# Kernel tuning notes

Measured on AMD Instinct MI355X. Metric: run time of the kernel, lower is better.

Reference implementation:

```python
import jax, jax.numpy as jnp
import numpy as np

EMBED = 1024
HEADS = 16
HEAD_DIM = EMBED // HEADS
LN_EPS = 1e-5


def setup_inputs() -> dict:
    key = jax.random.key(0)
    ks = jax.random.split(key, 12)
    B, LQ, LK = 2, 2048, 2048
    s = 1.0 / np.sqrt(EMBED)
    inp = {
        "query_seq": jax.random.normal(ks[0], (B, LQ, EMBED), jnp.float32),
        "key_value_seq": jax.random.normal(ks[1], (B, LK, EMBED), jnp.float32),
        "prompt_size": 0,
        "Wq": jax.random.normal(ks[2], (EMBED, EMBED), jnp.float32) * s,
        "bq": jnp.zeros((EMBED,), jnp.float32),
        "Wk": jax.random.normal(ks[3], (EMBED, EMBED), jnp.float32) * s,
        "bk": jnp.zeros((EMBED,), jnp.float32),
        "Wv": jax.random.normal(ks[4], (EMBED, EMBED), jnp.float32) * s,
        "bv": jnp.zeros((EMBED,), jnp.float32),
        "Wo": jax.random.normal(ks[5], (EMBED, EMBED), jnp.float32) * s,
        "bo": jnp.zeros((EMBED,), jnp.float32),
        "ln_gamma": jnp.ones((EMBED,), jnp.float32),
        "ln_beta": jnp.zeros((EMBED,), jnp.float32),
    }
    return inp


def _split_heads(x):
    B, L, _ = x.shape
    return x.reshape(B, L, HEADS, HEAD_DIM).transpose(0, 2, 1, 3)  # [B,H,L,Dh]


def reference(query_seq, key_value_seq, prompt_size, Wq, bq, Wk, bk, Wv, bv, Wo, bo, ln_gamma, ln_beta):
    # projections (torch nn.Linear: x @ W.T + b)
    q = _split_heads(query_seq @ Wq.T + bq)
    k = _split_heads(key_value_seq @ Wk.T + bk)
    v = _split_heads(key_value_seq @ Wv.T + bv)
    # naive attention: full score matrix, softmax over keys
    scores = jnp.einsum("bhqd,bhkd->bhqk", q, k) / np.sqrt(HEAD_DIM).astype(np.float32)
    attn = jax.nn.softmax(scores, axis=-1)
    ctx = jnp.einsum("bhqk,bhkd->bhqd", attn, v)
    B, H, LQ, Dh = ctx.shape
    ctx = ctx.transpose(0, 2, 1, 3).reshape(B, LQ, H * Dh)
    out = ctx @ Wo.T + bo
    # residual + LayerNorm
    x = out + query_seq
    mu = jnp.mean(x, axis=-1, keepdims=True)
    var = jnp.var(x, axis=-1, keepdims=True)
    return (x - mu) * jax.lax.rsqrt(var + LN_EPS) * ln_gamma + ln_beta
```

## Files before the change

kernel.cpp:

```cpp
#include <hip/hip_runtime.h>

typedef unsigned short u16;
typedef unsigned int u32;
typedef __attribute__((ext_vector_type(8))) __bf16 bf16x8;
typedef __attribute__((ext_vector_type(4))) short short4v;
typedef __attribute__((ext_vector_type(4))) float f32x4;
typedef __attribute__((ext_vector_type(16))) float f32x16;

#define EMBED 1024
#define NB 2
#define LQ 2048
#define HEADS 16
#define DH 64
#define QSCALE 0.18033688011112042f

__device__ __forceinline__ u16 f2bf(float f) {
  u32 u = __float_as_uint(f);
  u32 r = (u + 0x7FFFu + ((u >> 16) & 1u)) >> 16;
  return (u16)r;
}

__device__ __forceinline__ void glds16(const void* g, void* l) {
  __builtin_amdgcn_global_load_lds((const __attribute__((address_space(1))) void*)g,
                                   (__attribute__((address_space(3))) void*)l, 16, 0, 0);
}

__device__ __forceinline__ f32x4 mfma16(bf16x8 a, bf16x8 b, f32x4 c) {
  return __builtin_amdgcn_mfma_f32_16x16x32_bf16(a, b, c, 0, 0, 0);
}
__device__ __forceinline__ f32x16 mfma32(bf16x8 a, bf16x8 b, f32x16 c) {
  return __builtin_amdgcn_mfma_f32_32x32x16_bf16(a, b, c, 0, 0, 0);
}
__device__ __forceinline__ f32x16 mfma32x8(short4v a, short4v b, f32x16 c) {
  return __builtin_amdgcn_mfma_f32_32x32x8bf16_1k(a, b, c, 0, 0, 0);
}

__device__ __forceinline__ u32 packbf(float a, float b) {
  return __builtin_amdgcn_perm(__float_as_uint(b), __float_as_uint(a), 0x07060302u);
}

__global__ __launch_bounds__(256) void cast_kernel(
    const float* __restrict__ q, const float* __restrict__ kv,
    const float* __restrict__ wq, const float* __restrict__ wk,
    const float* __restrict__ wv, const float* __restrict__ wo,
    u16* __restrict__ qb, u16* __restrict__ kvb, u16* __restrict__ wqb,
    u16* __restrict__ wkb, u16* __restrict__ wvb, u16* __restrict__ wob) {
  int bid = blockIdx.x;
  const float* src;
  u16* dst;
  long base;
  if (bid < 2048) {
    src = q; dst = qb; base = (long)bid * 2048;
  } else if (bid < 4096) {
    src = kv; dst = kvb; base = (long)(bid - 2048) * 2048;
  } else {
    int wsel = (bid - 4096) >> 9;
    int wb = (bid - 4096) & 511;
    if (wsel == 0) { src = wq; dst = wqb; }
    else if (wsel == 1) { src = wk; dst = wkb; }
    else if (wsel == 2) { src = wv; dst = wvb; }
    else { src = wo; dst = wob; }
    base = (long)wb * 2048;
  }
  long e = base + (long)threadIdx.x * 8;
  float4 f0 = *(const float4*)(src + e);
  float4 f1 = *(const float4*)(src + e + 4);
  uint4 o;
  o.x = (u32)f2bf(f0.x) | ((u32)f2bf(f0.y) << 16);
  o.y = (u32)f2bf(f0.z) | ((u32)f2bf(f0.w) << 16);
  o.z = (u32)f2bf(f1.x) | ((u32)f2bf(f1.y) << 16);
  o.w = (u32)f2bf(f1.z) | ((u32)f2bf(f1.w) << 16);
  *(uint4*)(dst + e) = o;
}

template <int IT>
__device__ __forceinline__ void gemm_core(
    u16* As, u16* Bs, const u16* __restrict__ A, const u16* __restrict__ W,
    const float* __restrict__ bias, const float* __restrict__ resid,
    void* __restrict__ outp, int mode, int bx, int by) {
  const int K = EMBED;
  const int TM = IT * 32;
  const int tid = threadIdx.x;
  const int lane = tid & 63;
  const int wv = tid >> 6;
  const int wm = wv >> 1, wn = wv & 1;
  const int l16 = lane & 15, quad = lane >> 4;
  const long tile_m = (long)bx * TM;
  const long tile_n = (long)by * 128;

  f32x4 z4 = {0.f, 0.f, 0.f, 0.f};
  f32x4 acc[IT][4];
#pragma unroll
  for (int i = 0; i < IT; i++)
#pragma unroll
    for (int j = 0; j < 4; j++) acc[i][j] = z4;

  for (int k0 = 0; k0 < K; k0 += 64) {
#pragma unroll
    for (int it = 0; it < TM / 32; it++) {
      int lin = it * 256 + tid;
      int row = lin >> 3, cc = lin & 7;
      glds16(A + (tile_m + row) * K + k0 + ((cc ^ (row & 7)) << 3), As + lin * 8);
    }
#pragma unroll
    for (int it = 0; it < 4; it++) {
      int lin = it * 256 + tid;
      int row = lin >> 3, cc = lin & 7;
      glds16(W + (tile_n + row) * K + k0 + ((cc ^ (row & 7)) << 3), Bs + lin * 8);
    }
    __syncthreads();
    bf16x8 af[IT][2], bfr[4][2];
#pragma unroll
    for (int i = 0; i < IT; i++) {
      int row = wm * (IT * 16) + i * 16 + l16;
#pragma unroll
      for (int ki = 0; ki < 2; ki++)
        af[i][ki] = *(const bf16x8*)(As + row * 64 + (((ki * 4 + quad) ^ (row & 7)) << 3));
    }
#pragma unroll
    for (int j = 0; j < 4; j++) {
      int row = wn * 64 + j * 16 + l16;
#pragma unroll
      for (int ki = 0; ki < 2; ki++)
        bfr[j][ki] = *(const bf16x8*)(Bs + row * 64 + (((ki * 4 + quad) ^ (row & 7)) << 3));
    }
#pragma unroll
    for (int ki = 0; ki < 2; ki++)
#pragma unroll
      for (int i = 0; i < IT; i++)
#pragma unroll
        for (int j = 0; j < 4; j++) acc[i][j] = mfma16(af[i][ki], bfr[j][ki], acc[i][j]);
    __syncthreads();
  }

#pragma unroll
  for (int j = 0; j < 4; j++) {
    int gn = (int)tile_n + wn * 64 + j * 16 + l16;
    float bv = bias[gn];
#pragma unroll
    for (int i = 0; i < IT; i++) {
      long gm0 = tile_m + wm * (IT * 16) + i * 16 + quad * 4;
      if (mode == 3) {
#pragma unroll
        for (int r = 0; r < 4; r++) {
          long idx = (gm0 + r) * EMBED + gn;
          ((float*)outp)[idx] = acc[i][j][r] + bv + resid[idx];
        }
      } else if (mode == 2) {
        int b = (int)(gm0 >> 11), l = (int)(gm0 & 2047);
        int hh = gn >> 6, dh = gn & 63;
        uint2 pk;
        pk.x = (u32)f2bf(acc[i][j][0] + bv) | ((u32)f2bf(acc[i][j][1] + bv) << 16);
        pk.y = (u32)f2bf(acc[i][j][2] + bv) | ((u32)f2bf(acc[i][j][3] + bv) << 16);
        *(uint2*)((u16*)outp + (long)((b * HEADS + hh) * DH + dh) * LQ + l) = pk;
      } else {
#pragma unroll
        for (int r = 0; r < 4; r++) {
          long gm = gm0 + r;
          float v = acc[i][j][r] + bv;
          if (mode == 0) v *= QSCALE;
          int b = (int)(gm >> 11), l = (int)(gm & 2047);
          int hh = gn >> 6, dh = gn & 63;
          ((u16*)outp)[(long)((b * HEADS + hh) * LQ + l) * DH + dh] = f2bf(v);
        }
      }
    }
  }
}

__global__ __launch_bounds__(256) void qkv_kernel(
    const u16* __restrict__ qb, const u16* __restrict__ kvb,
    const u16* __restrict__ wqb, const u16* __restrict__ wkb, const u16* __restrict__ wvb,
    const float* __restrict__ bq, const float* __restrict__ bk, const float* __restrict__ bv,
    u16* __restrict__ Qh, u16* __restrict__ Kh, u16* __restrict__ Vt) {
  __shared__ u16 As[128 * 64];
  __shared__ u16 Bs[128 * 64];
  if (blockIdx.z == 0)      gemm_core<4>(As, Bs, qb,  wqb, bq, nullptr, Qh, 0, blockIdx.x, blockIdx.y);
  else if (blockIdx.z == 1) gemm_core<4>(As, Bs, kvb, wkb, bk, nullptr, Kh, 1, blockIdx.x, blockIdx.y);
  else                      gemm_core<4>(As, Bs, kvb, wvb, bv, nullptr, Vt, 2, blockIdx.x, blockIdx.y);
}

__global__ __launch_bounds__(256) void oproj_kernel(
    const u16* __restrict__ ctx, const u16* __restrict__ wob,
    const float* __restrict__ bo, const float* __restrict__ resid, float* __restrict__ out) {
  __shared__ u16 As[64 * 64];
  __shared__ u16 Bs[128 * 64];
  gemm_core<2>(As, Bs, ctx, wob, bo, resid, out, 3, blockIdx.x, blockIdx.y);
}

__global__ __launch_bounds__(256, 2) void attn_kernel(
    const u16* __restrict__ Qh, const u16* __restrict__ Kh,
    const u16* __restrict__ Vt, u16* __restrict__ ctx) {
  __shared__ u16 Qs[128 * 64];
  __shared__ u16 KVs[2][2][64 * 64];
  const int tid = threadIdx.x;
  const int lane = tid & 63;
  const int wv = tid >> 6;
  const int l32 = lane & 31, h = lane >> 5;
  const int qt = blockIdx.x, bh = blockIdx.y;
  const long qoff = (long)bh * (LQ * DH) + (long)qt * (128 * DH);
  const long koff = (long)bh * (LQ * DH);
  const long voff = (long)bh * (DH * LQ);
  const int qbase = wv * 32;

#pragma unroll
  for (int it = 0; it < 4; it++) {
    int lin = it * 256 + tid;
    int row = lin >> 3, cc = lin & 7;
    glds16(Qh + qoff + row * 64 + ((cc ^ (row & 7)) << 3), Qs + lin * 8);
  }
#pragma unroll
  for (int it = 0; it < 2; it++) {
    int lin = it * 256 + tid;
    int row = lin >> 3, cc = lin & 7;
    glds16(Kh + koff + (long)row * 64 + ((cc ^ (row & 7)) << 3), KVs[0][0] + lin * 8);
    glds16(Vt + voff + (long)row * LQ + ((cc ^ (row & 7)) << 3), KVs[0][1] + lin * 8);
  }
  __syncthreads();

  bf16x8 bq[4];
  {
    int row = qbase + l32;
#pragma unroll
    for (int ks = 0; ks < 4; ks++)
      bq[ks] = *(const bf16x8*)(Qs + row * 64 + (((ks * 2 + h) ^ (row & 7)) << 3));
  }

  f32x16 z16 = {0.f, 0.f, 0.f, 0.f, 0.f, 0.f, 0.f, 0.f,
                0.f, 0.f, 0.f, 0.f, 0.f, 0.f, 0.f, 0.f};
  f32x16 ot[2];
  ot[0] = z16;
  ot[1] = z16;
  float2 ls2 = {0.f, 0.f};

  for (int kt = 0; kt < 32; kt++) {
    const u16* Ks = KVs[kt & 1][0];
    const u16* Vts = KVs[kt & 1][1];
    if (kt + 1 < 32) {
      u16* Kn = (u16*)KVs[(kt + 1) & 1][0];
      u16* Vn = (u16*)KVs[(kt + 1) & 1][1];
#pragma unroll
      for (int it = 0; it < 2; it++) {
        int lin = it * 256 + tid;
        int row = lin >> 3, cc = lin & 7;
        glds16(Kh + koff + (long)((kt + 1) * 64 + row) * 64 + ((cc ^ (row & 7)) << 3), Kn + lin * 8);
        glds16(Vt + voff + (long)row * LQ + (kt + 1) * 64 + ((cc ^ (row & 7)) << 3), Vn + lin * 8);
      }
    }

    f32x16 st[2];
    st[0] = z16;
    st[1] = z16;
#pragma unroll
    for (int ks = 0; ks < 4; ks++) {
#pragma unroll
      for (int mt = 0; mt < 2; mt++) {
        int row = mt * 32 + l32;
        bf16x8 ak = *(const bf16x8*)(Ks + row * 64 + (((ks * 2 + h) ^ (row & 7)) << 3));
        st[mt] = mfma32(ak, bq[ks], st[mt]);
      }
    }

    uint2 pk[2][4];
#pragma unroll
    for (int mt = 0; mt < 2; mt++) {
#pragma unroll
      for (int g = 0; g < 4; g++) {
        float p0 = exp2f(st[mt][g * 4 + 0]);
        float p1 = exp2f(st[mt][g * 4 + 1]);
        float p2 = exp2f(st[mt][g * 4 + 2]);
        float p3 = exp2f(st[mt][g * 4 + 3]);
        float2 a = {p0, p1}, bb = {p2, p3};
        ls2.x += a.x + bb.x;
        ls2.y += a.y + bb.y;
        pk[mt][g].x = packbf(p0, p1);
        pk[mt][g].y = packbf(p2, p3);
      }
    }

#pragma unroll
    for (int t = 0; t < 8; t++) {
      short4v bp = *(short4v*)&pk[t >> 2][t & 3];
#pragma unroll
      for (int mt2 = 0; mt2 < 2; mt2++) {
        int row = mt2 * 32 + l32;
        short4v av = *(const short4v*)(Vts + row * 64 + (((t ^ (row & 7))) << 3) + 4 * h);
        ot[mt2] = mfma32x8(av, bp, ot[mt2]);
      }
    }
    __syncthreads();
  }

  float lsum = ls2.x + ls2.y;
  lsum += __shfl_xor(lsum, 32);
  float inv = 1.0f / lsum;

  const int b = bh >> 4, head = bh & 15;
  int qrow = qt * 128 + qbase + l32;
  long base = (long)(b * LQ + qrow) * EMBED + head * DH;
#pragma unroll
  for (int mt = 0; mt < 2; mt++) {
#pragma unroll
    for (int g = 0; g < 4; g++) {
      uint2 pkk;
      pkk.x = (u32)f2bf(ot[mt][g * 4 + 0] * inv) | ((u32)f2bf(ot[mt][g * 4 + 1] * inv) << 16);
      pkk.y = (u32)f2bf(ot[mt][g * 4 + 2] * inv) | ((u32)f2bf(ot[mt][g * 4 + 3] * inv) << 16);
      *(uint2*)(ctx + base + mt * 32 + g * 8 + 4 * h) = pkk;
    }
  }
}

__global__ __launch_bounds__(256) void ln_kernel(
    float* __restrict__ x, const float* __restrict__ gamma, const float* __restrict__ beta) {
  __shared__ float red[8];
  const int tid = threadIdx.x;
  const long row = blockIdx.x;
  float4 v = *(const float4*)(x + row * EMBED + tid * 4);
  float s = v.x + v.y + v.z + v.w;
  float sq = v.x * v.x + v.y * v.y + v.z * v.z + v.w * v.w;
#pragma unroll
  for (int off = 1; off < 64; off <<= 1) {
    s += __shfl_xor(s, off);
    sq += __shfl_xor(sq, off);
  }
  if ((tid & 63) == 0) {
    red[(tid >> 6) * 2] = s;
    red[(tid >> 6) * 2 + 1] = sq;
  }
  __syncthreads();
  s = red[0] + red[2] + red[4] + red[6];
  sq = red[1] + red[3] + red[5] + red[7];
  float mu = s * (1.f / EMBED);
  float var = sq * (1.f / EMBED) - mu * mu;
  float rstd = rsqrtf(var + 1e-5f);
  float4 g = *(const float4*)(gamma + tid * 4);
  float4 bt = *(const float4*)(beta + tid * 4);
  float4 ov;
  ov.x = (v.x - mu) * rstd * g.x + bt.x;
  ov.y = (v.y - mu) * rstd * g.y + bt.y;
  ov.z = (v.z - mu) * rstd * g.z + bt.z;
  ov.w = (v.w - mu) * rstd * g.w + bt.w;
  *(float4*)(x + row * EMBED + tid * 4) = ov;
}

extern "C" void kernel_launch(void* const* d_in, const int* in_sizes, int n_in,
                              void* d_out, int out_size, void* d_ws, size_t ws_size,
                              hipStream_t stream) {
  const float* q     = (const float*)d_in[0];
  const float* kv    = (const float*)d_in[1];
  const float* Wq    = (const float*)d_in[3];
  const float* bq    = (const float*)d_in[4];
  const float* Wk    = (const float*)d_in[5];
  const float* bk    = (const float*)d_in[6];
  const float* Wv    = (const float*)d_in[7];
  const float* bv    = (const float*)d_in[8];
  const float* Wo    = (const float*)d_in[9];
  const float* bo    = (const float*)d_in[10];
  const float* gamma = (const float*)d_in[11];
  const float* beta  = (const float*)d_in[12];

  char* ws = (char*)d_ws;
  u16* qb  = (u16*)(ws + (0l  << 20));
  u16* kvb = (u16*)(ws + (8l  << 20));
  u16* wqb = (u16*)(ws + (16l << 20));
  u16* wkb = (u16*)(ws + (18l << 20));
  u16* wvb = (u16*)(ws + (20l << 20));
  u16* wob = (u16*)(ws + (22l << 20));
  u16* Qh  = (u16*)(ws + (24l << 20));
  u16* Kh  = (u16*)(ws + (32l << 20));
  u16* Vt  = (u16*)(ws + (40l << 20));
  u16* ctx = (u16*)(ws + (48l << 20));
  float* out = (float*)d_out;

  cast_kernel<<<6144, 256, 0, stream>>>(q, kv, Wq, Wk, Wv, Wo, qb, kvb, wqb, wkb, wvb, wob);
  qkv_kernel<<<dim3(32, 8, 3), 256, 0, stream>>>(qb, kvb, wqb, wkb, wvb, bq, bk, bv, Qh, Kh, Vt);
  attn_kernel<<<dim3(16, 32), 256, 0, stream>>>(Qh, Kh, Vt, ctx);
  oproj_kernel<<<dim3(64, 8), 256, 0, stream>>>(ctx, wob, bo, q, out);
  ln_kernel<<<4096, 256, 0, stream>>>(out, gamma, beta);
}
```

Before: 242.5 us.

## Split attention over two key halves with a combine kernel for partial sums

Splits the key/value sequence across a new grid dimension so each attention block processes half the keys, writing unnormalized bf16 partial context and row sums; a new combine kernel adds the halves and normalizes. Q staging now reuses the KV shared buffer to cut LDS use, allowing launch bounds of four blocks per CU, and the PV accumulation is split into even/odd accumulators to break MFMA dependency chains. This doubles the grid to improve occupancy and CU fill, at the cost of an extra kernel launch, extra global traffic for partials, and extra bf16 rounding of unnormalized partials. It relies on the absence of a running max, since the two halves share one exponent scale.

```diff
diff --git a/kernel.cpp b/kernel.cpp
--- a/kernel.cpp
+++ b/kernel.cpp
@@ -188,21 +188,21 @@
   gemm_core<2>(As, Bs, ctx, wob, bo, resid, out, 3, blockIdx.x, blockIdx.y);
 }
 
-__global__ __launch_bounds__(256, 2) void attn_kernel(
+__global__ __launch_bounds__(256, 4) void attn_kernel(
     const u16* __restrict__ Qh, const u16* __restrict__ Kh,
-    const u16* __restrict__ Vt, u16* __restrict__ ctx) {
-  __shared__ u16 Qs[128 * 64];
+    const u16* __restrict__ Vt, u16* __restrict__ ctxp, float* __restrict__ lsump) {
   __shared__ u16 KVs[2][2][64 * 64];
   const int tid = threadIdx.x;
   const int lane = tid & 63;
   const int wv = tid >> 6;
   const int l32 = lane & 31, h = lane >> 5;
-  const int qt = blockIdx.x, bh = blockIdx.y;
+  const int qt = blockIdx.x, bh = blockIdx.y, kz = blockIdx.z;
   const long qoff = (long)bh * (LQ * DH) + (long)qt * (128 * DH);
-  const long koff = (long)bh * (LQ * DH);
-  const long voff = (long)bh * (DH * LQ);
+  const long koff = (long)bh * (LQ * DH) + (long)kz * (1024 * DH);
+  const long voff = (long)bh * (DH * LQ) + (long)kz * 1024;
   const int qbase = wv * 32;
 
+  u16* Qs = (u16*)KVs[1];
 #pragma unroll
   for (int it = 0; it < 4; it++) {
     int lin = it * 256 + tid;
@@ -225,18 +225,18 @@
     for (int ks = 0; ks < 4; ks++)
       bq[ks] = *(const bf16x8*)(Qs + row * 64 + (((ks * 2 + h) ^ (row & 7)) << 3));
   }
+  __syncthreads();
 
   f32x16 z16 = {0.f, 0.f, 0.f, 0.f, 0.f, 0.f, 0.f, 0.f,
                 0.f, 0.f, 0.f, 0.f, 0.f, 0.f, 0.f, 0.f};
-  f32x16 ot[2];
-  ot[0] = z16;
-  ot[1] = z16;
+  f32x16 ote[2], oto[2];
+  ote[0] = z16; ote[1] = z16; oto[0] = z16; oto[1] = z16;
   float2 ls2 = {0.f, 0.f};
 
-  for (int kt = 0; kt < 32; kt++) {
+  for (int kt = 0; kt < 16; kt++) {
     const u16* Ks = KVs[kt & 1][0];
     const u16* Vts = KVs[kt & 1][1];
-    if (kt + 1 < 32) {
+    if (kt + 1 < 16) {
       u16* Kn = (u16*)KVs[(kt + 1) & 1][0];
       u16* Vn = (u16*)KVs[(kt + 1) & 1][1];
 #pragma unroll
@@ -270,9 +270,8 @@
         float p1 = exp2f(st[mt][g * 4 + 1]);
         float p2 = exp2f(st[mt][g * 4 + 2]);
         float p3 = exp2f(st[mt][g * 4 + 3]);
-        float2 a = {p0, p1}, bb = {p2, p3};
-        ls2.x += a.x + bb.x;
-        ls2.y += a.y + bb.y;
+        ls2.x += p0 + p2;
+        ls2.y += p1 + p3;
         pk[mt][g].x = packbf(p0, p1);
         pk[mt][g].y = packbf(p2, p3);
       }
@@ -285,7 +284,8 @@
       for (int mt2 = 0; mt2 < 2; mt2++) {
         int row = mt2 * 32 + l32;
         short4v av = *(const short4v*)(Vts + row * 64 + (((t ^ (row & 7))) << 3) + 4 * h);
-        ot[mt2] = mfma32x8(av, bp, ot[mt2]);
+        if (t & 1) oto[mt2] = mfma32x8(av, bp, oto[mt2]);
+        else       ote[mt2] = mfma32x8(av, bp, ote[mt2]);
       }
     }
     __syncthreads();
@@ -293,21 +293,45 @@
 
   float lsum = ls2.x + ls2.y;
   lsum += __shfl_xor(lsum, 32);
-  float inv = 1.0f / lsum;
 
   const int b = bh >> 4, head = bh & 15;
   int qrow = qt * 128 + qbase + l32;
-  long base = (long)(b * LQ + qrow) * EMBED + head * DH;
+  if (h == 0) lsump[((long)kz * 32 + bh) * LQ + qrow] = lsum;
+  long base = (long)kz * (NB * LQ * EMBED) + (long)(b * LQ + qrow) * EMBED + head * DH;
 #pragma unroll
   for (int mt = 0; mt < 2; mt++) {
+    f32x16 ot = ote[mt] + oto[mt];
 #pragma unroll
     for (int g = 0; g < 4; g++) {
       uint2 pkk;
-      pkk.x = (u32)f2bf(ot[mt][g * 4 + 0] * inv) | ((u32)f2bf(ot[mt][g * 4 + 1] * inv) << 16);
-      pkk.y = (u32)f2bf(ot[mt][g * 4 + 2] * inv) | ((u32)f2bf(ot[mt][g * 4 + 3] * inv) << 16);
-      *(uint2*)(ctx + base + mt * 32 + g * 8 + 4 * h) = pkk;
-    }
-  }
+      pkk.x = (u32)f2bf(ot[g * 4 + 0]) | ((u32)f2bf(ot[g * 4 + 1]) << 16);
+      pkk.y = (u32)f2bf(ot[g * 4 + 2]) | ((u32)f2bf(ot[g * 4 + 3]) << 16);
+      *(uint2*)(ctxp + base + mt * 32 + g * 8 + 4 * h) = pkk;
+    }
+  }
+}
+
+__global__ __launch_bounds__(256) void combine_kernel(
+    const u16* __restrict__ ctxp, const float* __restrict__ lsump,
+    u16* __restrict__ ctx) {
+  const int m = blockIdx.x;
+  const int tid = threadIdx.x;
+  const int b = m >> 11, l = m & 2047;
+  const int head = tid >> 4;
+  float l0 = lsump[(long)(b * HEADS + head) * LQ + l];
+  float l1 = lsump[(long)(32 + b * HEADS + head) * LQ + l];
+  float inv = 1.0f / (l0 + l1);
+  long idx = (long)m * EMBED + tid * 4;
+  uint2 a = *(const uint2*)(ctxp + idx);
+  uint2 c = *(const uint2*)(ctxp + (long)(NB * LQ * EMBED) + idx);
+  float f0 = __uint_as_float(a.x << 16) + __uint_as_float(c.x << 16);
+  float f1 = __uint_as_float(a.x & 0xFFFF0000u) + __uint_as_float(c.x & 0xFFFF0000u);
+  float f2 = __uint_as_float(a.y << 16) + __uint_as_float(c.y << 16);
+  float f3 = __uint_as_float(a.y & 0xFFFF0000u) + __uint_as_float(c.y & 0xFFFF0000u);
+  uint2 o;
+  o.x = (u32)f2bf(f0 * inv) | ((u32)f2bf(f1 * inv) << 16);
+  o.y = (u32)f2bf(f2 * inv) | ((u32)f2bf(f3 * inv) << 16);
+  *(uint2*)(ctx + idx) = o;
 }
 
 __global__ __launch_bounds__(256) void ln_kernel(
@@ -360,21 +384,24 @@
   const float* beta  = (const float*)d_in[12];
 
   char* ws = (char*)d_ws;
-  u16* qb  = (u16*)(ws + (0l  << 20));
-  u16* kvb = (u16*)(ws + (8l  << 20));
-  u16* wqb = (u16*)(ws + (16l << 20));
-  u16* wkb = (u16*)(ws + (18l << 20));
-  u16* wvb = (u16*)(ws + (20l << 20));
-  u16* wob = (u16*)(ws + (22l << 20));
-  u16* Qh  = (u16*)(ws + (24l << 20));
-  u16* Kh  = (u16*)(ws + (32l << 20));
-  u16* Vt  = (u16*)(ws + (40l << 20));
-  u16* ctx = (u16*)(ws + (48l << 20));
+  u16* qb    = (u16*)(ws + (0l  << 20));
+  u16* kvb   = (u16*)(ws + (8l  << 20));
+  u16* wqb   = (u16*)(ws + (16l << 20));
+  u16* wkb   = (u16*)(ws + (18l << 20));
+  u16* wvb   = (u16*)(ws + (20l << 20));
+  u16* wob   = (u16*)(ws + (22l << 20));
+  u16* Qh    = (u16*)(ws + (24l << 20));
+  u16* Kh    = (u16*)(ws + (32l << 20));
+  u16* Vt    = (u16*)(ws + (40l << 20));
+  u16* ctxp  = (u16*)(ws + (48l << 20));
+  float* lsump = (float*)(ws + (0l << 20));
+  u16* ctx   = (u16*)(ws + (24l << 20));
   float* out = (float*)d_out;
 
   cast_kernel<<<6144, 256, 0, stream>>>(q, kv, Wq, Wk, Wv, Wo, qb, kvb, wqb, wkb, wvb, wob);
   qkv_kernel<<<dim3(32, 8, 3), 256, 0, stream>>>(qb, kvb, wqb, wkb, wvb, bq, bk, bv, Qh, Kh, Vt);
-  attn_kernel<<<dim3(16, 32), 256, 0, stream>>>(Qh, Kh, Vt, ctx);
+  attn_kernel<<<dim3(16, 32, 2), 256, 0, stream>>>(Qh, Kh, Vt, ctxp, lsump);
+  combine_kernel<<<4096, 256, 0, stream>>>(ctxp, lsump, ctx);
   oproj_kernel<<<dim3(64, 8), 256, 0, stream>>>(ctx, wob, bo, q, out);
   ln_kernel<<<4096, 256, 0, stream>>>(out, gamma, beta);
 }
```

After: 307.4 us. 1.27x slower.
